# Kernel optimization log

Hardware: AMD Instinct MI355X
Metric: run time of the kernel (lower is better)

The kernel has to match this reference:

```python
import jax, jax.numpy as jnp
import numpy as np

N, E, D, H = 50000, 800000, 128, 4
DH = D // H  # head dim = 32


def setup_inputs() -> dict:
    key = jax.random.key(0)
    ks = jax.random.split(key, 16)
    inp = {
        "node_feats": jax.random.normal(ks[0], (N, D), jnp.float32),
        "edge_feats": jax.random.normal(ks[1], (E, D), jnp.float32),
        "src": jax.random.randint(ks[2], (E,), 0, N, jnp.int32),
        "dst": jax.random.randint(ks[3], (E,), 0, N, jnp.int32),
        # MHA projections (no bias since num_input == num_output feats)
        "Wq": jax.random.normal(ks[4], (D, D), jnp.float32) / np.sqrt(D),
        "Wk": jax.random.normal(ks[5], (D, D), jnp.float32) / np.sqrt(D),
        "Wv": jax.random.normal(ks[6], (D, D), jnp.float32) / np.sqrt(D),
        "We": jax.random.normal(ks[7], (D, D), jnp.float32) / np.sqrt(D),
        # output projection (with bias)
        "O_w": jax.random.normal(ks[8], (D, D), jnp.float32) / np.sqrt(D),
        "O_b": jnp.zeros((D,), jnp.float32),
        # batch-norm affine params
        "g1n": jnp.ones((D,), jnp.float32), "b1n": jnp.zeros((D,), jnp.float32),
        "g1e": jnp.ones((D,), jnp.float32), "b1e": jnp.zeros((D,), jnp.float32),
        "g2": jnp.ones((D,), jnp.float32), "b2": jnp.zeros((D,), jnp.float32),
        # node-feats MLP (no bias)
        "W1": jax.random.normal(ks[9], (D, 2 * D), jnp.float32) / np.sqrt(D),
        "W2": jax.random.normal(ks[10], (2 * D, D), jnp.float32) / np.sqrt(2 * D),
    }
    return inp


def _batch_norm(x, gamma, beta, eps=1e-5):
    # training-style BatchNorm1d: biased variance over the batch (node/edge) dim
    mean = jnp.mean(x, axis=0)
    var = jnp.var(x, axis=0)
    return (x - mean) * jax.lax.rsqrt(var + eps) * gamma + beta


def reference(node_feats, edge_feats, src, dst, Wq, Wk, Wv, We, O_w, O_b,
              g1n, b1n, g1e, b1e, g2, b2, W1, W2):
    h_in1 = node_feats
    nf = _batch_norm(node_feats, g1n, b1n)
    ef = _batch_norm(edge_feats, g1e, b1e)

    Q = (nf @ Wq).reshape(N, H, DH)
    K = (nf @ Wk).reshape(N, H, DH)
    V = (nf @ Wv).reshape(N, H, DH)
    proj_e = (ef @ We).reshape(E, H, DH)

    # edge-wise multiplicative attention: [E, H, DH]
    score = jnp.clip(K[src] * Q[dst] / np.sqrt(DH).astype(np.float32), -5.0, 5.0) * proj_e
    s = jnp.exp(jnp.clip(jnp.sum(score, axis=-1, keepdims=True), -5.0, 5.0))  # [E, H, 1]

    # scatter-sum aggregation to destination nodes
    wV = jax.ops.segment_sum(s * V[src], dst, num_segments=N)  # [N, H, DH]
    z = jax.ops.segment_sum(s, dst, num_segments=N)            # [N, H, 1]
    h = (wV / (z + 1e-6)).reshape(N, D)

    # dropout is identity in eval mode
    h = h @ O_w + O_b
    h = h_in1 + h  # residual 1

    h_in2 = h
    h = _batch_norm(h, g2, b2)
    h = jax.nn.silu(h @ W1) @ W2  # node_feats_MLP (dropout = identity)
    h = h_in2 + h  # residual 2
    return h
```

## Files before the change

kernel.cpp:

```cpp
#include <hip/hip_runtime.h>
#include <hip/hip_bf16.h>
#include <math.h>

#define N_NODES 50000
#define N_EDGES 800000
#define DIM 128
#define NH 4

typedef __attribute__((ext_vector_type(8))) short bf16x8;
typedef __attribute__((ext_vector_type(4))) float f32x4;
typedef unsigned int uint;
typedef unsigned short ushort;

__device__ inline short f2bf(float f) {
  __hip_bfloat16 h = __float2bfloat16(f);
  return __builtin_bit_cast(short, h);
}
__device__ inline uint pack_bf2(float lo, float hi) {
  return (uint)(ushort)f2bf(lo) | ((uint)(ushort)f2bf(hi) << 16);
}
__device__ inline float bflo(uint u) { return __builtin_bit_cast(float, u << 16); }
__device__ inline float bfhi(uint u) { return __builtin_bit_cast(float, u & 0xffff0000u); }

__global__ __launch_bounds__(256) void bn_stats_kernel(
    const float* __restrict__ x, int M, float* __restrict__ out) {
  __shared__ float s_sum[DIM];
  __shared__ float s_sq[DIM];
  int t = threadIdx.x;
  if (t < DIM) { s_sum[t] = 0.f; s_sq[t] = 0.f; }
  __syncthreads();
  int c4 = (t & 31) * 4;
  int rg = t >> 5;
  float sum0=0,sum1=0,sum2=0,sum3=0, sq0=0,sq1=0,sq2=0,sq3=0;
  for (long row = (long)blockIdx.x * 8 + rg; row < M; row += (long)gridDim.x * 8) {
    float4 v = *reinterpret_cast<const float4*>(x + row * DIM + c4);
    sum0 += v.x; sq0 += v.x * v.x;
    sum1 += v.y; sq1 += v.y * v.y;
    sum2 += v.z; sq2 += v.z * v.z;
    sum3 += v.w; sq3 += v.w * v.w;
  }
  atomicAdd(&s_sum[c4 + 0], sum0); atomicAdd(&s_sq[c4 + 0], sq0);
  atomicAdd(&s_sum[c4 + 1], sum1); atomicAdd(&s_sq[c4 + 1], sq1);
  atomicAdd(&s_sum[c4 + 2], sum2); atomicAdd(&s_sq[c4 + 2], sq2);
  atomicAdd(&s_sum[c4 + 3], sum3); atomicAdd(&s_sq[c4 + 3], sq3);
  __syncthreads();
  if (t < DIM) {
    atomicAdd(&out[t], s_sum[t]);
    atomicAdd(&out[DIM + t], s_sq[t]);
  }
}

__global__ __launch_bounds__(128) void finalize2_kernel(
    const float* __restrict__ stats_n, const float* __restrict__ stats_e,
    const float* __restrict__ g1n, const float* __restrict__ b1n,
    const float* __restrict__ g1e, const float* __restrict__ b1e,
    float* __restrict__ ab_n, float* __restrict__ ab_e) {
  int t = threadIdx.x;
  const float* stats = blockIdx.x ? stats_e : stats_n;
  const float* gamma = blockIdx.x ? g1e : g1n;
  const float* beta  = blockIdx.x ? b1e : b1n;
  float* ab          = blockIdx.x ? ab_e : ab_n;
  float M            = blockIdx.x ? (float)N_EDGES : (float)N_NODES;
  float mean = stats[t] / M;
  float var = stats[DIM + t] / M - mean * mean;
  float a = gamma[t] * rsqrtf(var + 1e-5f);
  ab[t] = a;
  ab[DIM + t] = beta[t] - mean * a;
}

__global__ __launch_bounds__(128) void finalize_ab_kernel(
    const float* __restrict__ stats, float M,
    const float* __restrict__ gamma, const float* __restrict__ beta,
    float* __restrict__ ab) {
  int t = threadIdx.x;
  float mean = stats[t] / M;
  float var = stats[DIM + t] / M - mean * mean;
  float a = gamma[t] * rsqrtf(var + 1e-5f);
  ab[t] = a;
  ab[DIM + t] = beta[t] - mean * a;
}

__global__ __launch_bounds__(1024) void fold4_kernel(
    const float* __restrict__ Wq, const float* __restrict__ Wk,
    const float* __restrict__ Wv, const float* __restrict__ We,
    const float* __restrict__ ab_n, const float* __restrict__ ab_e, float inv_s,
    short* __restrict__ WqT, short* __restrict__ WkT,
    short* __restrict__ WvT, short* __restrict__ WeT,
    float* __restrict__ bq, float* __restrict__ bk,
    float* __restrict__ bv, float* __restrict__ be) {
  __shared__ float red[8][DIM];
  int b = blockIdx.x;
  const float* W = (b == 0) ? Wq : (b == 1) ? Wk : (b == 2) ? Wv : We;
  const float* ab = (b == 3) ? ab_e : ab_n;
  float scale = (b == 1) ? inv_s : 1.f;
  short* WT = (b == 0) ? WqT : (b == 1) ? WkT : (b == 2) ? WvT : WeT;
  float* bias = (b == 0) ? bq : (b == 1) ? bk : (b == 2) ? bv : be;
  int t = threadIdx.x;
  int d = t & 127, kg = t >> 7;
  int ct = d >> 4, lr = d & 15;
  int L = (ct >> 1) * 32 + lr * 2 + (ct & 1);
  float bacc = 0.f;
#pragma unroll
  for (int j = 0; j < 16; ++j) {
    int k = kg * 16 + j;
    float wv = W[k * DIM + L];
    WT[d * DIM + k] = f2bf(scale * ab[k] * wv);
    bacc += ab[DIM + k] * wv;
  }
  red[kg][d] = bacc;
  __syncthreads();
  if (kg == 0) {
    float s = 0.f;
#pragma unroll
    for (int j = 0; j < 8; ++j) s += red[j][d];
    bias[d] = scale * s;
  }
}

__global__ __launch_bounds__(256) void fold_static_kernel(
    const float* __restrict__ Ow, const float* __restrict__ W2,
    short* __restrict__ OwT, short* __restrict__ W2T) {
  int t = threadIdx.x;
  int d = t & 127, kh = t >> 7;
  if (blockIdx.x == 0) {
    for (int j = 0; j < 64; ++j) {
      int k = kh * 64 + j;
      OwT[d * DIM + k] = f2bf(Ow[k * DIM + d]);
    }
  } else {
    for (int j = 0; j < 128; ++j) {
      int k = kh * 128 + j;
      W2T[d * 256 + k] = f2bf(W2[k * DIM + d]);
    }
  }
}

__global__ __launch_bounds__(256) void fold_w1_kernel(
    const float* __restrict__ W1, const float* __restrict__ ab2,
    short* __restrict__ W1F, float* __restrict__ bias1) {
  int d = threadIdx.x;
  float bacc = 0.f;
  for (int k = 0; k < DIM; ++k) {
    float wv = W1[k * 256 + d];
    W1F[d * DIM + k] = f2bf(ab2[k] * wv);
    bacc += ab2[DIM + k] * wv;
  }
  bias1[d] = bacc;
}

__device__ inline void load_a_frags(const float* __restrict__ X, long m0,
                                    int lr, int lg, bf16x8 a[4]) {
#pragma unroll
  for (int ks = 0; ks < 4; ++ks) {
    const float* p = X + (m0 + lr) * DIM + ks * 32 + lg * 8;
    float4 v0 = *reinterpret_cast<const float4*>(p);
    float4 v1 = *reinterpret_cast<const float4*>(p + 4);
    bf16x8 af;
    af[0] = f2bf(v0.x); af[1] = f2bf(v0.y); af[2] = f2bf(v0.z); af[3] = f2bf(v0.w);
    af[4] = f2bf(v1.x); af[5] = f2bf(v1.y); af[6] = f2bf(v1.z); af[7] = f2bf(v1.w);
    a[ks] = af;
  }
}

__global__ __launch_bounds__(256) void qkv_mfma_kernel(
    const float* __restrict__ nf,
    const short* __restrict__ WqT, const short* __restrict__ WkT, const short* __restrict__ WvT,
    const float* __restrict__ bq, const float* __restrict__ bk, const float* __restrict__ bv,
    ushort* __restrict__ Qb, ushort* __restrict__ Kb, ushort* __restrict__ Vb) {
  int t = threadIdx.x;
  int w = t >> 6, l = t & 63;
  int lr = l & 15, lg = l >> 4;
  long m0 = (long)blockIdx.x * 64 + w * 16;
  if (m0 >= N_NODES) return;
  bf16x8 a[4];
  load_a_frags(nf, m0, lr, lg, a);
  const short* Ws[3] = {WqT, WkT, WvT};
  const float* bs[3] = {bq, bk, bv};
  ushort* Os[3] = {Qb, Kb, Vb};
#pragma unroll 1
  for (int m = 0; m < 3; ++m) {
    const short* WT = Ws[m];
    f32x4 acc[8];
#pragma unroll
    for (int ct = 0; ct < 8; ++ct) acc[ct] = (f32x4){0.f, 0.f, 0.f, 0.f};
#pragma unroll
    for (int ct = 0; ct < 8; ++ct) {
#pragma unroll
      for (int ks = 0; ks < 4; ++ks) {
        bf16x8 b = *reinterpret_cast<const bf16x8*>(WT + (ct * 16 + lr) * DIM + ks * 32 + lg * 8);
        acc[ct] = __builtin_amdgcn_mfma_f32_16x16x32_bf16(a[ks], b, acc[ct], 0, 0, 0);
      }
    }
    const float* bb = bs[m];
    ushort* O = Os[m];
#pragma unroll
    for (int h = 0; h < 4; ++h) {
      float b0 = bb[(2 * h) * 16 + lr];
      float b1 = bb[(2 * h + 1) * 16 + lr];
#pragma unroll
      for (int r = 0; r < 4; ++r) {
        uint u = pack_bf2(acc[2 * h][r] + b0, acc[2 * h + 1][r] + b1);
        *reinterpret_cast<uint*>(O + (m0 + lg * 4 + r) * DIM + h * 32 + lr * 2) = u;
      }
    }
  }
}

__global__ __launch_bounds__(256) void hist_kernel(
    const int* __restrict__ dst, int* __restrict__ deg) {
  int i = blockIdx.x * 256 + threadIdx.x;
  atomicAdd(&deg[dst[i]], 1);
}

#define SCAN_T 1024
#define PER_T 49
__global__ __launch_bounds__(SCAN_T) void scan_kernel(
    const int* __restrict__ deg, int* __restrict__ row_start, int* __restrict__ cursor) {
  __shared__ int ps[SCAN_T];
  int t = threadIdx.x;
  int base = t * PER_T;
  int lsum = 0;
  int local[PER_T];
#pragma unroll
  for (int j = 0; j < PER_T; ++j) {
    int idx = base + j;
    int d = (idx < N_NODES) ? deg[idx] : 0;
    local[j] = lsum;
    lsum += d;
  }
  ps[t] = lsum;
  __syncthreads();
  for (int off = 1; off < SCAN_T; off <<= 1) {
    int v = (t >= off) ? ps[t - off] : 0;
    __syncthreads();
    ps[t] += v;
    __syncthreads();
  }
  int prefix = (t == 0) ? 0 : ps[t - 1];
#pragma unroll
  for (int j = 0; j < PER_T; ++j) {
    int idx = base + j;
    if (idx < N_NODES) {
      int v = prefix + local[j];
      row_start[idx] = v;
      cursor[idx] = v;
    }
  }
  if (t == SCAN_T - 1) row_start[N_NODES] = ps[SCAN_T - 1];
}

__global__ __launch_bounds__(256) void scatter_kernel(
    const int* __restrict__ src, const int* __restrict__ dst,
    int* __restrict__ cursor, int2* __restrict__ csr) {
  int i = blockIdx.x * 256 + threadIdx.x;
  int d = dst[i];
  int pos = atomicAdd(&cursor[d], 1);
  csr[pos] = make_int2(src[i], i);
}

#define ES_GRID 1024
__global__ __launch_bounds__(256) void edge_score_kernel(
    const float* __restrict__ ef,
    const int* __restrict__ src, const int* __restrict__ dst,
    const short* __restrict__ WeT, const float* __restrict__ be,
    const ushort* __restrict__ Qb, const ushort* __restrict__ Kb,
    float* __restrict__ s_out) {
  const int NT = N_EDGES / 64;
  int t = threadIdx.x;
  int w = t >> 6, l = t & 63;
  int lr = l & 15, lg = l >> 4;
  int stride = gridDim.x;
  float ber[8];
#pragma unroll
  for (int ct = 0; ct < 8; ++ct) ber[ct] = be[ct * 16 + lr];

  int tile = blockIdx.x;
  int4 s4, d4;
  f32x4 af[8];
  {
    long m0 = (long)tile * 64 + w * 16;
    long eb = m0 + lg * 4;
    s4 = *reinterpret_cast<const int4*>(src + eb);
    d4 = *reinterpret_cast<const int4*>(dst + eb);
#pragma unroll
    for (int ks = 0; ks < 4; ++ks) {
      const float* p = ef + (m0 + lr) * DIM + ks * 32 + lg * 8;
      af[2 * ks]     = __builtin_nontemporal_load(reinterpret_cast<const f32x4*>(p));
      af[2 * ks + 1] = __builtin_nontemporal_load(reinterpret_cast<const f32x4*>(p + 4));
    }
  }

#pragma unroll 2
  for (; tile < NT; tile += stride) {
    int pt = (tile + stride < NT) ? (tile + stride) : (NT - 1);
    int sn[4] = {s4.x, s4.y, s4.z, s4.w};
    int dn[4] = {d4.x, d4.y, d4.z, d4.w};
    uint Kg[4][4], Qg[4][4];
#pragma unroll
    for (int r = 0; r < 4; ++r) {
#pragma unroll
      for (int h = 0; h < 4; ++h) {
        Kg[r][h] = *reinterpret_cast<const uint*>(Kb + (long)sn[r] * DIM + h * 32 + lr * 2);
        Qg[r][h] = *reinterpret_cast<const uint*>(Qb + (long)dn[r] * DIM + h * 32 + lr * 2);
      }
    }
    long pm0 = (long)pt * 64 + w * 16;
    long peb = pm0 + lg * 4;
    int4 ns4 = *reinterpret_cast<const int4*>(src + peb);
    int4 nd4 = *reinterpret_cast<const int4*>(dst + peb);
    bf16x8 a[4];
#pragma unroll
    for (int ks = 0; ks < 4; ++ks) {
      f32x4 v0 = af[2 * ks], v1 = af[2 * ks + 1];
      bf16x8 t8;
      t8[0] = f2bf(v0.x); t8[1] = f2bf(v0.y); t8[2] = f2bf(v0.z); t8[3] = f2bf(v0.w);
      t8[4] = f2bf(v1.x); t8[5] = f2bf(v1.y); t8[6] = f2bf(v1.z); t8[7] = f2bf(v1.w);
      a[ks] = t8;
    }
    f32x4 naf[8];
#pragma unroll
    for (int ks = 0; ks < 4; ++ks) {
      const float* p = ef + (pm0 + lr) * DIM + ks * 32 + lg * 8;
      naf[2 * ks]     = __builtin_nontemporal_load(reinterpret_cast<const f32x4*>(p));
      naf[2 * ks + 1] = __builtin_nontemporal_load(reinterpret_cast<const f32x4*>(p + 4));
    }
    f32x4 acc[8];
#pragma unroll
    for (int ct = 0; ct < 8; ++ct) acc[ct] = (f32x4){0.f, 0.f, 0.f, 0.f};
#pragma unroll
    for (int ct = 0; ct < 8; ++ct) {
#pragma unroll
      for (int ks = 0; ks < 4; ++ks) {
        bf16x8 b = *reinterpret_cast<const bf16x8*>(WeT + (ct * 16 + lr) * DIM + ks * 32 + lg * 8);
        acc[ct] = __builtin_amdgcn_mfma_f32_16x16x32_bf16(a[ks], b, acc[ct], 0, 0, 0);
      }
    }
    long eb = (long)tile * 64 + w * 16 + lg * 4;
#pragma unroll
    for (int r = 0; r < 4; ++r) {
      float hs0, hs1, hs2, hs3;
      {
        float h0, h1, h2, h3;
#pragma unroll
        for (int h = 0; h < 4; ++h) {
          float k0 = bflo(Kg[r][h]), k1 = bfhi(Kg[r][h]);
          float q0 = bflo(Qg[r][h]), q1 = bfhi(Qg[r][h]);
          float pe0 = acc[2 * h][r] + ber[2 * h];
          float pe1 = acc[2 * h + 1][r] + ber[2 * h + 1];
          float v = fminf(fmaxf(k0 * q0, -5.f), 5.f) * pe0
                  + fminf(fmaxf(k1 * q1, -5.f), 5.f) * pe1;
          if (h == 0) h0 = v; else if (h == 1) h1 = v; else if (h == 2) h2 = v; else h3 = v;
        }
        hs0 = h0; hs1 = h1; hs2 = h2; hs3 = h3;
      }
#pragma unroll
      for (int m2 = 8; m2 >= 1; m2 >>= 1) {
        hs0 += __shfl_xor(hs0, m2);
        hs1 += __shfl_xor(hs1, m2);
        hs2 += __shfl_xor(hs2, m2);
        hs3 += __shfl_xor(hs3, m2);
      }
      if (lr < 4) {
        float myh = (lr == 0) ? hs0 : ((lr == 1) ? hs1 : ((lr == 2) ? hs2 : hs3));
        s_out[(eb + r) * 4 + lr] = __expf(fminf(fmaxf(myh, -5.f), 5.f));
      }
    }
    s4 = ns4; d4 = nd4;
#pragma unroll
    for (int i = 0; i < 8; ++i) af[i] = naf[i];
  }
}

__global__ __launch_bounds__(256) void aggregate_kernel(
    const int* __restrict__ row_start, const int2* __restrict__ csr,
    const float* __restrict__ s_arr, const ushort* __restrict__ Vb,
    float* __restrict__ hagg) {
  int t = threadIdx.x;
  int w = t >> 6, l = t & 63;
  int n = blockIdx.x * 4 + w;
  int r0 = row_start[n], r1 = row_start[n + 1];
  int h = l >> 4;
  float a0 = 0.f, a1 = 0.f, zacc = 0.f;
  int idx = r0;
  for (; idx + 2 <= r1; idx += 2) {
    int2 ra = csr[idx];
    int2 rb = csr[idx + 1];
    float sa = s_arr[(long)ra.y * 4 + h];
    float sb = s_arr[(long)rb.y * 4 + h];
    uint ua = *reinterpret_cast<const uint*>(Vb + (long)ra.x * DIM + l * 2);
    uint ub = *reinterpret_cast<const uint*>(Vb + (long)rb.x * DIM + l * 2);
    a0 += sa * bflo(ua) + sb * bflo(ub);
    a1 += sa * bfhi(ua) + sb * bfhi(ub);
    zacc += sa + sb;
  }
  if (idx < r1) {
    int2 ra = csr[idx];
    float sa = s_arr[(long)ra.y * 4 + h];
    uint ua = *reinterpret_cast<const uint*>(Vb + (long)ra.x * DIM + l * 2);
    a0 += sa * bflo(ua);
    a1 += sa * bfhi(ua);
    zacc += sa;
  }
  float inv = 1.f / (zacc + 1e-6f);
  float2 o; o.x = a0 * inv; o.y = a1 * inv;
  *reinterpret_cast<float2*>(hagg + (long)n * DIM + l * 2) = o;
}

__global__ __launch_bounds__(256) void attnout_mfma_kernel(
    const float* __restrict__ hagg, const short* __restrict__ OwT,
    const float* __restrict__ Ob, const float* __restrict__ h_in1,
    float* __restrict__ hres, float* __restrict__ stats2) {
  int t = threadIdx.x;
  int w = t >> 6, l = t & 63;
  int lr = l & 15, lg = l >> 4;
  long m0 = (long)blockIdx.x * 64 + w * 16;
  if (m0 >= N_NODES) return;
  bf16x8 a[4];
  load_a_frags(hagg, m0, lr, lg, a);
  f32x4 acc[8];
#pragma unroll
  for (int ct = 0; ct < 8; ++ct) acc[ct] = (f32x4){0.f, 0.f, 0.f, 0.f};
#pragma unroll
  for (int ct = 0; ct < 8; ++ct) {
#pragma unroll
    for (int ks = 0; ks < 4; ++ks) {
      bf16x8 b = *reinterpret_cast<const bf16x8*>(OwT + (ct * 16 + lr) * DIM + ks * 32 + lg * 8);
      acc[ct] = __builtin_amdgcn_mfma_f32_16x16x32_bf16(a[ks], b, acc[ct], 0, 0, 0);
    }
  }
#pragma unroll
  for (int ct = 0; ct < 8; ++ct) {
    float ob = Ob[ct * 16 + lr];
    float ls = 0.f, lq = 0.f;
#pragma unroll
    for (int r = 0; r < 4; ++r) {
      long idx = (m0 + lg * 4 + r) * DIM + ct * 16 + lr;
      float hv = h_in1[idx] + acc[ct][r] + ob;
      hres[idx] = hv;
      ls += hv; lq += hv * hv;
    }
    ls += __shfl_xor(ls, 16); ls += __shfl_xor(ls, 32);
    lq += __shfl_xor(lq, 16); lq += __shfl_xor(lq, 32);
    if (lg == 0) {
      atomicAdd(&stats2[ct * 16 + lr], ls);
      atomicAdd(&stats2[DIM + ct * 16 + lr], lq);
    }
  }
}

__global__ __launch_bounds__(256) void mlp_mfma_kernel(
    const float* __restrict__ hres, const short* __restrict__ W1F,
    const float* __restrict__ bias1, const short* __restrict__ W2T,
    float* __restrict__ out) {
  __shared__ short mid[64][264];
  int t = threadIdx.x;
  int w = t >> 6, l = t & 63;
  int lr = l & 15, lg = l >> 4;
  long m0 = (long)blockIdx.x * 64 + w * 16;
  if (m0 >= N_NODES) return;
  bf16x8 a1[4];
  load_a_frags(hres, m0, lr, lg, a1);
#pragma unroll
  for (int ct = 0; ct < 16; ++ct) {
    f32x4 acc = (f32x4){0.f, 0.f, 0.f, 0.f};
#pragma unroll
    for (int ks = 0; ks < 4; ++ks) {
      bf16x8 b = *reinterpret_cast<const bf16x8*>(W1F + (ct * 16 + lr) * DIM + ks * 32 + lg * 8);
      acc = __builtin_amdgcn_mfma_f32_16x16x32_bf16(a1[ks], b, acc, 0, 0, 0);
    }
    float bb = bias1[ct * 16 + lr];
#pragma unroll
    for (int r = 0; r < 4; ++r) {
      float x = acc[r] + bb;
      float sl = x / (1.f + __expf(-x));
      mid[w * 16 + lg * 4 + r][ct * 16 + lr] = f2bf(sl);
    }
  }
  bf16x8 a2[8];
#pragma unroll
  for (int ks = 0; ks < 8; ++ks) {
    a2[ks] = *reinterpret_cast<const bf16x8*>(&mid[w * 16 + lr][ks * 32 + lg * 8]);
  }
#pragma unroll
  for (int ct = 0; ct < 8; ++ct) {
    f32x4 acc = (f32x4){0.f, 0.f, 0.f, 0.f};
#pragma unroll
    for (int ks = 0; ks < 8; ++ks) {
      bf16x8 b = *reinterpret_cast<const bf16x8*>(W2T + (ct * 16 + lr) * 256 + ks * 32 + lg * 8);
      acc = __builtin_amdgcn_mfma_f32_16x16x32_bf16(a2[ks], b, acc, 0, 0, 0);
    }
#pragma unroll
    for (int r = 0; r < 4; ++r) {
      long idx = (m0 + lg * 4 + r) * DIM + ct * 16 + lr;
      out[idx] = hres[idx] + acc[r];
    }
  }
}

extern "C" void kernel_launch(void* const* d_in, const int* in_sizes, int n_in,
                              void* d_out, int out_size, void* d_ws, size_t ws_size,
                              hipStream_t stream) {
  const float* node_feats = (const float*)d_in[0];
  const float* edge_feats = (const float*)d_in[1];
  const int* src = (const int*)d_in[2];
  const int* dst = (const int*)d_in[3];
  const float* Wq = (const float*)d_in[4];
  const float* Wk = (const float*)d_in[5];
  const float* Wv = (const float*)d_in[6];
  const float* We = (const float*)d_in[7];
  const float* Ow = (const float*)d_in[8];
  const float* Ob = (const float*)d_in[9];
  const float* g1n = (const float*)d_in[10];
  const float* b1n = (const float*)d_in[11];
  const float* g1e = (const float*)d_in[12];
  const float* b1e = (const float*)d_in[13];
  const float* g2 = (const float*)d_in[14];
  const float* b2 = (const float*)d_in[15];
  const float* W1 = (const float*)d_in[16];
  const float* W2 = (const float*)d_in[17];
  float* out = (float*)d_out;
  float* w = (float*)d_ws;

  float* stats_n = w + 0;
  float* stats_e = w + 256;
  float* stats_h = w + 512;
  float* ab_n = w + 768;
  float* ab_e = w + 1024;
  float* ab_2 = w + 1280;
  float* bq = w + 1536;
  float* bk = w + 1664;
  float* bv = w + 1792;
  float* be = w + 1920;
  short* WqT = (short*)(w + 2048);
  short* WkT = (short*)(w + 10240);
  short* WvT = (short*)(w + 18432);
  short* WeT = (short*)(w + 26624);
  short* OwT = (short*)(w + 34816);
  short* W1F = (short*)(w + 43008);
  short* W2T = (short*)(w + 59392);
  float* bias1 = w + 75776;
  ushort* Qb = (ushort*)(w + 76032);
  ushort* Kb = (ushort*)(w + 3276032);
  ushort* Vb = (ushort*)(w + 6476032);
  float* s_arr = w + 9676032;
  int* deg = (int*)(w + 12876032);
  int* row_start = deg + 50048;
  int* cursor = row_start + 50064;
  int2* csr = (int2*)(cursor + 50048);
  float* hagg = w + 76032;

  const float inv_s = 0.17677669529663687f;

  hipMemsetAsync(w, 0, 768 * sizeof(float), stream);
  hipMemsetAsync(deg, 0, 50000 * sizeof(int), stream);

  bn_stats_kernel<<<512, 256, 0, stream>>>(node_feats, N_NODES, stats_n);
  bn_stats_kernel<<<2048, 256, 0, stream>>>(edge_feats, N_EDGES, stats_e);
  finalize2_kernel<<<2, 128, 0, stream>>>(stats_n, stats_e, g1n, b1n, g1e, b1e, ab_n, ab_e);
  fold4_kernel<<<4, 1024, 0, stream>>>(Wq, Wk, Wv, We, ab_n, ab_e, inv_s,
                                       WqT, WkT, WvT, WeT, bq, bk, bv, be);
  fold_static_kernel<<<2, 256, 0, stream>>>(Ow, W2, OwT, W2T);

  hist_kernel<<<N_EDGES / 256, 256, 0, stream>>>(dst, deg);
  scan_kernel<<<1, SCAN_T, 0, stream>>>(deg, row_start, cursor);
  scatter_kernel<<<N_EDGES / 256, 256, 0, stream>>>(src, dst, cursor, csr);

  qkv_mfma_kernel<<<(N_NODES + 63) / 64, 256, 0, stream>>>(
      node_feats, WqT, WkT, WvT, bq, bk, bv, Qb, Kb, Vb);
  edge_score_kernel<<<ES_GRID, 256, 0, stream>>>(
      edge_feats, src, dst, WeT, be, Qb, Kb, s_arr);
  aggregate_kernel<<<N_NODES / 4, 256, 0, stream>>>(row_start, csr, s_arr, Vb, hagg);
  attnout_mfma_kernel<<<(N_NODES + 63) / 64, 256, 0, stream>>>(
      hagg, OwT, Ob, node_feats, out, stats_h);
  finalize_ab_kernel<<<1, 128, 0, stream>>>(stats_h, (float)N_NODES, g2, b2, ab_2);
  fold_w1_kernel<<<1, 256, 0, stream>>>(W1, ab_2, W1F, bias1);
  mlp_mfma_kernel<<<(N_NODES + 63) / 64, 256, 0, stream>>>(out, W1F, bias1, W2T, out);
}
```

Measured before the change: 808.9 us.

## Fuse small setup kernels, store aggregated features as bf16, unroll aggregation

Merges the degree histogram into the edge batch-norm stats kernel and folds the BN finalize and static weight transposes into one fold kernel. The second BN finalize is moved into fold_w1, which cuts several tiny launches. The aggregate kernel now unrolls by 4 to keep more gathers in flight and writes bf16 output, so the output projection loads bf16 fragments directly and reads half the bytes. The edge score grid is doubled. The change adds bf16 rounding of the aggregated features before the output projection, though these were already converted to bf16 for the MFMA.

```diff
diff --git a/kernel.cpp b/kernel.cpp
--- a/kernel.cpp
+++ b/kernel.cpp
@@ -50,52 +50,88 @@
   }
 }
 
-__global__ __launch_bounds__(128) void finalize2_kernel(
+__global__ __launch_bounds__(256) void bn_stats_hist_kernel(
+    const float* __restrict__ x, const int* __restrict__ dst,
+    float* __restrict__ out, int* __restrict__ deg) {
+  __shared__ float s_sum[DIM];
+  __shared__ float s_sq[DIM];
+  int t = threadIdx.x;
+  if (t < DIM) { s_sum[t] = 0.f; s_sq[t] = 0.f; }
+  __syncthreads();
+  for (long i = (long)blockIdx.x * 256 + t; i < N_EDGES; i += (long)gridDim.x * 256) {
+    atomicAdd(&deg[dst[i]], 1);
+  }
+  int c4 = (t & 31) * 4;
+  int rg = t >> 5;
+  float sum0=0,sum1=0,sum2=0,sum3=0, sq0=0,sq1=0,sq2=0,sq3=0;
+  for (long row = (long)blockIdx.x * 8 + rg; row < N_EDGES; row += (long)gridDim.x * 8) {
+    float4 v = *reinterpret_cast<const float4*>(x + row * DIM + c4);
+    sum0 += v.x; sq0 += v.x * v.x;
+    sum1 += v.y; sq1 += v.y * v.y;
+    sum2 += v.z; sq2 += v.z * v.z;
+    sum3 += v.w; sq3 += v.w * v.w;
+  }
+  atomicAdd(&s_sum[c4 + 0], sum0); atomicAdd(&s_sq[c4 + 0], sq0);
+  atomicAdd(&s_sum[c4 + 1], sum1); atomicAdd(&s_sq[c4 + 1], sq1);
+  atomicAdd(&s_sum[c4 + 2], sum2); atomicAdd(&s_sq[c4 + 2], sq2);
+  atomicAdd(&s_sum[c4 + 3], sum3); atomicAdd(&s_sq[c4 + 3], sq3);
+  __syncthreads();
+  if (t < DIM) {
+    atomicAdd(&out[t], s_sum[t]);
+    atomicAdd(&out[DIM + t], s_sq[t]);
+  }
+}
+
+__global__ __launch_bounds__(1024) void fold6_kernel(
+    const float* __restrict__ Wq, const float* __restrict__ Wk,
+    const float* __restrict__ Wv, const float* __restrict__ We,
+    const float* __restrict__ Ow, const float* __restrict__ W2,
     const float* __restrict__ stats_n, const float* __restrict__ stats_e,
     const float* __restrict__ g1n, const float* __restrict__ b1n,
-    const float* __restrict__ g1e, const float* __restrict__ b1e,
-    float* __restrict__ ab_n, float* __restrict__ ab_e) {
-  int t = threadIdx.x;
-  const float* stats = blockIdx.x ? stats_e : stats_n;
-  const float* gamma = blockIdx.x ? g1e : g1n;
-  const float* beta  = blockIdx.x ? b1e : b1n;
-  float* ab          = blockIdx.x ? ab_e : ab_n;
-  float M            = blockIdx.x ? (float)N_EDGES : (float)N_NODES;
-  float mean = stats[t] / M;
-  float var = stats[DIM + t] / M - mean * mean;
-  float a = gamma[t] * rsqrtf(var + 1e-5f);
-  ab[t] = a;
-  ab[DIM + t] = beta[t] - mean * a;
-}
-
-__global__ __launch_bounds__(128) void finalize_ab_kernel(
-    const float* __restrict__ stats, float M,
-    const float* __restrict__ gamma, const float* __restrict__ beta,
-    float* __restrict__ ab) {
-  int t = threadIdx.x;
-  float mean = stats[t] / M;
-  float var = stats[DIM + t] / M - mean * mean;
-  float a = gamma[t] * rsqrtf(var + 1e-5f);
-  ab[t] = a;
-  ab[DIM + t] = beta[t] - mean * a;
-}
-
-__global__ __launch_bounds__(1024) void fold4_kernel(
-    const float* __restrict__ Wq, const float* __restrict__ Wk,
-    const float* __restrict__ Wv, const float* __restrict__ We,
-    const float* __restrict__ ab_n, const float* __restrict__ ab_e, float inv_s,
+    const float* __restrict__ g1e, const float* __restrict__ b1e, float inv_s,
     short* __restrict__ WqT, short* __restrict__ WkT,
     short* __restrict__ WvT, short* __restrict__ WeT,
+    short* __restrict__ OwT, short* __restrict__ W2T,
     float* __restrict__ bq, float* __restrict__ bk,
     float* __restrict__ bv, float* __restrict__ be) {
+  int b = blockIdx.x;
+  int t = threadIdx.x;
+  if (b == 4) {
+    int d = t & 127, kg = t >> 7;
+#pragma unroll
+    for (int j = 0; j < 16; ++j) {
+      int k = kg * 16 + j;
+      OwT[d * DIM + k] = f2bf(Ow[k * DIM + d]);
+    }
+    return;
+  }
+  if (b == 5) {
+    int d = t & 127, kg = t >> 7;
+#pragma unroll
+    for (int j = 0; j < 32; ++j) {
+      int k = kg * 32 + j;
+      W2T[d * 256 + k] = f2bf(W2[k * DIM + d]);
+    }
+    return;
+  }
   __shared__ float red[8][DIM];
-  int b = blockIdx.x;
+  __shared__ float sab[DIM], sbb[DIM];
   const float* W = (b == 0) ? Wq : (b == 1) ? Wk : (b == 2) ? Wv : We;
-  const float* ab = (b == 3) ? ab_e : ab_n;
+  const float* stats = (b == 3) ? stats_e : stats_n;
+  const float* gamma = (b == 3) ? g1e : g1n;
+  const float* beta  = (b == 3) ? b1e : b1n;
+  float M            = (b == 3) ? (float)N_EDGES : (float)N_NODES;
   float scale = (b == 1) ? inv_s : 1.f;
   short* WT = (b == 0) ? WqT : (b == 1) ? WkT : (b == 2) ? WvT : WeT;
   float* bias = (b == 0) ? bq : (b == 1) ? bk : (b == 2) ? bv : be;
-  int t = threadIdx.x;
+  if (t < DIM) {
+    float mean = stats[t] / M;
+    float var = stats[DIM + t] / M - mean * mean;
+    float a = gamma[t] * rsqrtf(var + 1e-5f);
+    sab[t] = a;
+    sbb[t] = beta[t] - mean * a;
+  }
+  __syncthreads();
   int d = t & 127, kg = t >> 7;
   int ct = d >> 4, lr = d & 15;
   int L = (ct >> 1) * 32 + lr * 2 + (ct & 1);
@@ -104,8 +140,8 @@
   for (int j = 0; j < 16; ++j) {
     int k = kg * 16 + j;
     float wv = W[k * DIM + L];
-    WT[d * DIM + k] = f2bf(scale * ab[k] * wv);
-    bacc += ab[DIM + k] * wv;
+    WT[d * DIM + k] = f2bf(scale * sab[k] * wv);
+    bacc += sbb[k] * wv;
   }
   red[kg][d] = bacc;
   __syncthreads();
@@ -117,35 +153,27 @@
   }
 }
 
-__global__ __launch_bounds__(256) void fold_static_kernel(
-    const float* __restrict__ Ow, const float* __restrict__ W2,
-    short* __restrict__ OwT, short* __restrict__ W2T) {
-  int t = threadIdx.x;
-  int d = t & 127, kh = t >> 7;
-  if (blockIdx.x == 0) {
-    for (int j = 0; j < 64; ++j) {
-      int k = kh * 64 + j;
-      OwT[d * DIM + k] = f2bf(Ow[k * DIM + d]);
-    }
-  } else {
-    for (int j = 0; j < 128; ++j) {
-      int k = kh * 128 + j;
-      W2T[d * 256 + k] = f2bf(W2[k * DIM + d]);
-    }
-  }
-}
-
 __global__ __launch_bounds__(256) void fold_w1_kernel(
-    const float* __restrict__ W1, const float* __restrict__ ab2,
+    const float* __restrict__ W1, const float* __restrict__ stats_h,
+    const float* __restrict__ g2, const float* __restrict__ b2,
     short* __restrict__ W1F, float* __restrict__ bias1) {
-  int d = threadIdx.x;
+  __shared__ float sab[DIM], sbb[DIM];
+  int t = threadIdx.x;
+  if (t < DIM) {
+    float mean = stats_h[t] / (float)N_NODES;
+    float var = stats_h[DIM + t] / (float)N_NODES - mean * mean;
+    float a = g2[t] * rsqrtf(var + 1e-5f);
+    sab[t] = a;
+    sbb[t] = b2[t] - mean * a;
+  }
+  __syncthreads();
   float bacc = 0.f;
   for (int k = 0; k < DIM; ++k) {
-    float wv = W1[k * 256 + d];
-    W1F[d * DIM + k] = f2bf(ab2[k] * wv);
-    bacc += ab2[DIM + k] * wv;
-  }
-  bias1[d] = bacc;
+    float wv = W1[k * 256 + t];
+    W1F[t * DIM + k] = f2bf(sab[k] * wv);
+    bacc += sbb[k] * wv;
+  }
+  bias1[t] = bacc;
 }
 
 __device__ inline void load_a_frags(const float* __restrict__ X, long m0,
@@ -206,12 +234,6 @@
   }
 }
 
-__global__ __launch_bounds__(256) void hist_kernel(
-    const int* __restrict__ dst, int* __restrict__ deg) {
-  int i = blockIdx.x * 256 + threadIdx.x;
-  atomicAdd(&deg[dst[i]], 1);
-}
-
 #define SCAN_T 1024
 #define PER_T 49
 __global__ __launch_bounds__(SCAN_T) void scan_kernel(
@@ -258,7 +280,7 @@
   csr[pos] = make_int2(src[i], i);
 }
 
-#define ES_GRID 1024
+#define ES_GRID 2048
 __global__ __launch_bounds__(256) void edge_score_kernel(
     const float* __restrict__ ef,
     const int* __restrict__ src, const int* __restrict__ dst,
@@ -374,7 +396,7 @@
 __global__ __launch_bounds__(256) void aggregate_kernel(
     const int* __restrict__ row_start, const int2* __restrict__ csr,
     const float* __restrict__ s_arr, const ushort* __restrict__ Vb,
-    float* __restrict__ hagg) {
+    ushort* __restrict__ haggb) {
   int t = threadIdx.x;
   int w = t >> 6, l = t & 63;
   int n = blockIdx.x * 4 + w;
@@ -382,18 +404,24 @@
   int h = l >> 4;
   float a0 = 0.f, a1 = 0.f, zacc = 0.f;
   int idx = r0;
-  for (; idx + 2 <= r1; idx += 2) {
-    int2 ra = csr[idx];
-    int2 rb = csr[idx + 1];
-    float sa = s_arr[(long)ra.y * 4 + h];
-    float sb = s_arr[(long)rb.y * 4 + h];
-    uint ua = *reinterpret_cast<const uint*>(Vb + (long)ra.x * DIM + l * 2);
-    uint ub = *reinterpret_cast<const uint*>(Vb + (long)rb.x * DIM + l * 2);
-    a0 += sa * bflo(ua) + sb * bflo(ub);
-    a1 += sa * bfhi(ua) + sb * bfhi(ub);
-    zacc += sa + sb;
-  }
-  if (idx < r1) {
+  for (; idx + 4 <= r1; idx += 4) {
+    int2 rec[4];
+#pragma unroll
+    for (int j = 0; j < 4; ++j) rec[j] = csr[idx + j];
+    float sv[4]; uint uv[4];
+#pragma unroll
+    for (int j = 0; j < 4; ++j) {
+      sv[j] = s_arr[(long)rec[j].y * 4 + h];
+      uv[j] = *reinterpret_cast<const uint*>(Vb + (long)rec[j].x * DIM + l * 2);
+    }
+#pragma unroll
+    for (int j = 0; j < 4; ++j) {
+      a0 += sv[j] * bflo(uv[j]);
+      a1 += sv[j] * bfhi(uv[j]);
+      zacc += sv[j];
+    }
+  }
+  for (; idx < r1; ++idx) {
     int2 ra = csr[idx];
     float sa = s_arr[(long)ra.y * 4 + h];
     uint ua = *reinterpret_cast<const uint*>(Vb + (long)ra.x * DIM + l * 2);
@@ -402,12 +430,11 @@
     zacc += sa;
   }
   float inv = 1.f / (zacc + 1e-6f);
-  float2 o; o.x = a0 * inv; o.y = a1 * inv;
-  *reinterpret_cast<float2*>(hagg + (long)n * DIM + l * 2) = o;
+  *reinterpret_cast<uint*>(haggb + (long)n * DIM + l * 2) = pack_bf2(a0 * inv, a1 * inv);
 }
 
 __global__ __launch_bounds__(256) void attnout_mfma_kernel(
-    const float* __restrict__ hagg, const short* __restrict__ OwT,
+    const ushort* __restrict__ haggb, const short* __restrict__ OwT,
     const float* __restrict__ Ob, const float* __restrict__ h_in1,
     float* __restrict__ hres, float* __restrict__ stats2) {
   int t = threadIdx.x;
@@ -416,7 +443,10 @@
   long m0 = (long)blockIdx.x * 64 + w * 16;
   if (m0 >= N_NODES) return;
   bf16x8 a[4];
-  load_a_frags(hagg, m0, lr, lg, a);
+#pragma unroll
+  for (int ks = 0; ks < 4; ++ks) {
+    a[ks] = *reinterpret_cast<const bf16x8*>(haggb + (m0 + lr) * DIM + ks * 32 + lg * 8);
+  }
   f32x4 acc[8];
 #pragma unroll
   for (int ct = 0; ct < 8; ++ct) acc[ct] = (f32x4){0.f, 0.f, 0.f, 0.f};
@@ -524,9 +554,6 @@
   float* stats_n = w + 0;
   float* stats_e = w + 256;
   float* stats_h = w + 512;
-  float* ab_n = w + 768;
-  float* ab_e = w + 1024;
-  float* ab_2 = w + 1280;
   float* bq = w + 1536;
   float* bk = w + 1664;
   float* bv = w + 1792;
@@ -547,7 +574,7 @@
   int* row_start = deg + 50048;
   int* cursor = row_start + 50064;
   int2* csr = (int2*)(cursor + 50048);
-  float* hagg = w + 76032;
+  ushort* haggb = (ushort*)(w + 76032);
 
   const float inv_s = 0.17677669529663687f;
 
@@ -555,13 +582,10 @@
   hipMemsetAsync(deg, 0, 50000 * sizeof(int), stream);
 
   bn_stats_kernel<<<512, 256, 0, stream>>>(node_feats, N_NODES, stats_n);
-  bn_stats_kernel<<<2048, 256, 0, stream>>>(edge_feats, N_EDGES, stats_e);
-  finalize2_kernel<<<2, 128, 0, stream>>>(stats_n, stats_e, g1n, b1n, g1e, b1e, ab_n, ab_e);
-  fold4_kernel<<<4, 1024, 0, stream>>>(Wq, Wk, Wv, We, ab_n, ab_e, inv_s,
-                                       WqT, WkT, WvT, WeT, bq, bk, bv, be);
-  fold_static_kernel<<<2, 256, 0, stream>>>(Ow, W2, OwT, W2T);
-
-  hist_kernel<<<N_EDGES / 256, 256, 0, stream>>>(dst, deg);
+  bn_stats_hist_kernel<<<2048, 256, 0, stream>>>(edge_feats, dst, stats_e, deg);
+  fold6_kernel<<<6, 1024, 0, stream>>>(Wq, Wk, Wv, We, Ow, W2, stats_n, stats_e,
+                                       g1n, b1n, g1e, b1e, inv_s,
+                                       WqT, WkT, WvT, WeT, OwT, W2T, bq, bk, bv, be);
   scan_kernel<<<1, SCAN_T, 0, stream>>>(deg, row_start, cursor);
   scatter_kernel<<<N_EDGES / 256, 256, 0, stream>>>(src, dst, cursor, csr);
 
@@ -569,10 +593,9 @@
       node_feats, WqT, WkT, WvT, bq, bk, bv, Qb, Kb, Vb);
   edge_score_kernel<<<ES_GRID, 256, 0, stream>>>(
       edge_feats, src, dst, WeT, be, Qb, Kb, s_arr);
-  aggregate_kernel<<<N_NODES / 4, 256, 0, stream>>>(row_start, csr, s_arr, Vb, hagg);
+  aggregate_kernel<<<N_NODES / 4, 256, 0, stream>>>(row_start, csr, s_arr, Vb, haggb);
   attnout_mfma_kernel<<<(N_NODES + 63) / 64, 256, 0, stream>>>(
-      hagg, OwT, Ob, node_feats, out, stats_h);
-  finalize_ab_kernel<<<1, 128, 0, stream>>>(stats_h, (float)N_NODES, g2, b2, ab_2);
-  fold_w1_kernel<<<1, 256, 0, stream>>>(W1, ab_2, W1F, bias1);
+      haggb, OwT, Ob, node_feats, out, stats_h);
+  fold_w1_kernel<<<1, 256, 0, stream>>>(W1, stats_h, g2, b2, W1F, bias1);
   mlp_mfma_kernel<<<(N_NODES + 63) / 64, 256, 0, stream>>>(out, W1F, bias1, W2T, out);
 }
```

New measurement: 814.4 us. About the same (+0.7%).
